# Kernel tuning notes

Hardware: AMD Instinct MI355X
Metric: run time of the kernel (lower is better)

The kernel has to match this reference:

```python
import jax, jax.numpy as jnp
import numpy as np

D_MODEL = 4096
N_HEADS = 32
N_KV_HEADS = 32
D_HEAD = 128
D_LATENT = 512
N_CKV = 4            # n_compressed_kv_heads = d_latent // d_head
T = 2048             # num_tokens (single-sequence prefill)
ROPE_BASE = 10000.0
NEG = -1e30


def _rope(x, positions):
    """Neox-style rotary embedding. x: (T, H, D)."""
    d = x.shape[-1]
    inv_freq = 1.0 / (ROPE_BASE ** (jnp.arange(0, d // 2, dtype=jnp.float32) * (2.0 / d)))
    freqs = positions.astype(jnp.float32)[:, None] * inv_freq[None, :]  # (T, D/2)
    cos = jnp.cos(freqs)[:, None, :]
    sin = jnp.sin(freqs)[:, None, :]
    x1, x2 = jnp.split(x, 2, axis=-1)
    return jnp.concatenate([x1 * cos - x2 * sin, x2 * cos + x1 * sin], axis=-1)


def setup_inputs() -> dict:
    key = jax.random.key(0)
    ks = jax.random.split(key, 6)
    s = jnp.float32(0.02)
    return {
        "positions": jnp.arange(T, dtype=jnp.int32),
        "hidden_states": jax.random.normal(ks[0], (T, D_MODEL), jnp.float32),
        "Wq": jax.random.normal(ks[1], (D_MODEL, N_HEADS * D_HEAD), jnp.float32) * s,
        "Wc": jax.random.normal(ks[2], (D_MODEL, 2 * D_LATENT), jnp.float32) * s,
        "Wuk": jax.random.normal(ks[3], (2 * D_LATENT, N_KV_HEADS * D_HEAD), jnp.float32) * s,
        "Wuv": jax.random.normal(ks[4], (2 * D_LATENT, N_KV_HEADS * D_HEAD), jnp.float32) * s,
        "Wo": jax.random.normal(ks[5], (N_HEADS * D_HEAD, D_MODEL), jnp.float32) * s,
    }


def reference(positions, hidden_states, Wq, Wc, Wuk, Wuv, Wo):
    # Q projection
    q = (hidden_states @ Wq).reshape(T, N_HEADS, D_HEAD)
    # MLA compression: hidden -> c_kv (2*d_latent), split into c_k / c_v
    c_kv = hidden_states @ Wc                                   # (T, 2*D_LATENT)
    c_k = c_kv[:, :D_LATENT].reshape(T, N_CKV, D_HEAD)          # compressed K cache
    c_v = c_kv[:, D_LATENT:].reshape(T, N_CKV, D_HEAD)          # compressed V cache
    # Decompression (computed by the source module; K is RoPE'd then discarded,
    # V is unused -- the v1 attention path runs over the compressed cache).
    K = (c_kv @ Wuk).reshape(T, N_KV_HEADS, D_HEAD)
    V = (c_kv @ Wuv).reshape(T, N_KV_HEADS, D_HEAD)             # noqa: unused, matches source
    # RoPE on q (and K, whose rotated value is dead in the source)
    q = _rope(q, positions)
    K = _rope(K, positions)  # dead, kept for FLOP parity with the source
    # GQA attention: n_heads=32 query heads over n_compressed_kv_heads=4 kv heads
    g = N_HEADS // N_CKV
    qg = q.reshape(T, N_CKV, g, D_HEAD)
    scale = jnp.float32(1.0 / np.sqrt(D_HEAD))
    scores = jnp.einsum('tkgd,skd->kgts', qg, c_k) * scale      # (N_CKV, g, T, T)
    causal = positions[:, None] >= positions[None, :]           # (T, T)
    scores = jnp.where(causal[None, None], scores, NEG)
    probs = jax.nn.softmax(scores, axis=-1)
    ctx = jnp.einsum('kgts,skd->tkgd', probs, c_v).reshape(T, N_HEADS * D_HEAD)
    return ctx @ Wo
```

## Files before the change

### kernel.cpp

```cpp
#include <hip/hip_runtime.h>
#include <hip/hip_bf16.h>
#include <cstdint>
#include <cstddef>


typedef unsigned short u16;
typedef short s16x8 __attribute__((ext_vector_type(8)));
typedef short s16x4 __attribute__((ext_vector_type(4)));
typedef float f32x4 __attribute__((ext_vector_type(4)));

#define MFMA16(a, b, c) __builtin_amdgcn_mfma_f32_16x16x32_bf16((a), (b), (c), 0, 0, 0)

#define QSCALE 0.12751899f
#define LOG2_ROPE_BASE 13.287712379549449f
#define FIXMAX 24.0f

__device__ __forceinline__ u16 f2b(float f) {
  return __builtin_bit_cast(u16, __float2bfloat16(f));
}
__device__ __forceinline__ void async_copy16(u16* lds, const u16* g) {
  __builtin_amdgcn_global_load_lds(
      (const __attribute__((address_space(1))) unsigned int*)g,
      (__attribute__((address_space(3))) unsigned int*)lds, 16, 0, 0);
}

__global__ __launch_bounds__(256)
void prep_kernel(const float* __restrict__ hidden, const float* __restrict__ Wq,
                 const float* __restrict__ Wc, const float* __restrict__ Wo,
                 u16* __restrict__ hb, u16* __restrict__ WqT,
                 u16* __restrict__ WcT, u16* __restrict__ WoT) {
  __shared__ alignas(16) u16 tile[64 * 72];
  const int b = blockIdx.x;
  const int t = threadIdx.x;

  if (b >= 9216) {
    int i = (b - 9216) * 256 + t;
    const float4* p = (const float4*)hidden + (size_t)i * 2;
    float4 a = p[0], c = p[1];
    s16x8 v;
    v[0] = (short)f2b(a.x); v[1] = (short)f2b(a.y);
    v[2] = (short)f2b(a.z); v[3] = (short)f2b(a.w);
    v[4] = (short)f2b(c.x); v[5] = (short)f2b(c.y);
    v[6] = (short)f2b(c.z); v[7] = (short)f2b(c.w);
    *(s16x8*)&hb[(size_t)i * 8] = v;
    return;
  }

  const float* in;
  u16* out;
  int gx, in_ld, out_ld;
  if (b < 4096)      { in = Wq; out = WqT; gx = b;        in_ld = 4096; out_ld = 4096; }
  else if (b < 5120) { in = Wc; out = WcT; gx = b - 4096; in_ld = 1024; out_ld = 4096; }
  else               { in = Wo; out = WoT; gx = b - 5120; in_ld = 4096; out_ld = 4096; }
  const int nbx = in_ld / 64;
  const int c0 = (gx % nbx) * 64, r0 = (gx / nbx) * 64;
  const int rr = t >> 3, cc = (t & 7) * 8;
#pragma unroll
  for (int p = 0; p < 2; p++) {
    int row = p * 32 + rr;
    const float4* src = (const float4*)&in[(size_t)(r0 + row) * in_ld + c0 + cc];
    float4 a = src[0], c = src[1];
    s16x8 v;
    v[0] = (short)f2b(a.x); v[1] = (short)f2b(a.y);
    v[2] = (short)f2b(a.z); v[3] = (short)f2b(a.w);
    v[4] = (short)f2b(c.x); v[5] = (short)f2b(c.y);
    v[6] = (short)f2b(c.z); v[7] = (short)f2b(c.w);
    *(s16x8*)&tile[row * 72 + cc] = v;
  }
  __syncthreads();
#pragma unroll
  for (int p = 0; p < 2; p++) {
    int orow = p * 32 + rr;
    s16x8 v;
#pragma unroll
    for (int j = 0; j < 8; j++) v[j] = (short)tile[(cc + j) * 72 + orow];
    *(s16x8*)&out[(size_t)(c0 + orow) * out_ld + r0 + cc] = v;
  }
}

__global__ __launch_bounds__(256)
void transpose_ckv(const u16* __restrict__ in, u16* __restrict__ out) {
  __shared__ alignas(16) u16 tile[64 * 72];
  const int kh = blockIdx.z;
  const int c0 = blockIdx.x * 64, r0 = blockIdx.y * 64;
  const int in_off = 512 + kh * 128;
  u16* outk = out + (size_t)kh * 128 * 2048;
  const int t = threadIdx.x;
  const int rr = t >> 3, cc = (t & 7) * 8;
#pragma unroll
  for (int p = 0; p < 2; p++) {
    int row = p * 32 + rr;
    s16x8 v = *(const s16x8*)&in[(size_t)(r0 + row) * 1024 + in_off + c0 + cc];
    *(s16x8*)&tile[row * 72 + cc] = v;
  }
  __syncthreads();
#pragma unroll
  for (int p = 0; p < 2; p++) {
    int orow = p * 32 + rr;
    s16x8 v;
#pragma unroll
    for (int j = 0; j < 8; j++) v[j] = (short)tile[(cc + j) * 72 + orow];
    *(s16x8*)&outk[(size_t)(c0 + orow) * 2048 + r0 + cc] = v;
  }
}

template <int EPI>
__global__ __launch_bounds__(256, (EPI == 3) ? 4 : 3)
void gemm_bt(const u16* __restrict__ A, const u16* __restrict__ Bt,
             void* __restrict__ Cv, void* __restrict__ Cv2,
             const int* __restrict__ positions, int kHalf) {
  __shared__ alignas(16) u16 As[128 * 32];
  __shared__ alignas(16) u16 Bs[128 * 32];

  const int tid = threadIdx.x;
  const int w = tid >> 6, l = tid & 63;
  const int wm = w >> 1, wn = w & 1;
  const int lrow = l >> 4, lcol = l & 15;
  const int m0 = blockIdx.y * 128, n0 = blockIdx.x * 128;
  const int k0 = (EPI == 3) ? (int)blockIdx.z * kHalf : 0;
  const int k1 = (EPI == 3) ? k0 + kHalf : 4096;

  f32x4 acc[4][4] = {};

  const int srow = l >> 2;
  const int scol = (l & 3) * 8;
  const u16* Ag = A + (size_t)(m0 + w * 32 + srow) * 4096 + scol;
  const u16* Bg = Bt + (size_t)(n0 + w * 32 + srow) * 4096 + scol;

  for (int kt = k0; kt < k1; kt += 32) {
    __syncthreads();
    async_copy16(&As[(w * 32) * 32], Ag + kt);
    async_copy16(&As[(w * 32 + 16) * 32], Ag + (size_t)16 * 4096 + kt);
    async_copy16(&Bs[(w * 32) * 32], Bg + kt);
    async_copy16(&Bs[(w * 32 + 16) * 32], Bg + (size_t)16 * 4096 + kt);
    __syncthreads();

    s16x8 a[4], b[4];
#pragma unroll
    for (int i = 0; i < 4; i++)
      a[i] = *(const s16x8*)&As[(wm * 64 + i * 16 + lcol) * 32 + lrow * 8];
#pragma unroll
    for (int j = 0; j < 4; j++)
      b[j] = *(const s16x8*)&Bs[(wn * 32 + (j & 1) * 16 + (j >> 1) * 64 + lcol) * 32 +
                                lrow * 8];
#pragma unroll
    for (int i = 0; i < 4; i++)
#pragma unroll
      for (int j = 0; j < 4; j++)
        acc[i][j] = MFMA16(a[i], b[j], acc[i][j]);
  }

  if constexpr (EPI == 3) {
    float* C = (float*)Cv;
#pragma unroll
    for (int i = 0; i < 4; i++) {
      int row = m0 + wm * 64 + i * 16 + lrow * 4;
#pragma unroll
      for (int j = 0; j < 4; j++) {
        int col = n0 + wn * 32 + (j & 1) * 16 + (j >> 1) * 64 + lcol;
#pragma unroll
        for (int r = 0; r < 4; r++)
          atomicAdd(&C[(size_t)(row + r) * 4096 + col], acc[i][j][r]);
      }
    }
  } else {
    if (n0 >= 4096) {
      u16* C = (u16*)Cv2;
      int cb = n0 - 4096;
#pragma unroll
      for (int i = 0; i < 4; i++) {
        int row = m0 + wm * 64 + i * 16 + lrow * 4;
#pragma unroll
        for (int j = 0; j < 4; j++) {
          int col = cb + wn * 32 + (j & 1) * 16 + (j >> 1) * 64 + lcol;
#pragma unroll
          for (int r = 0; r < 4; r++)
            C[(size_t)(row + r) * 1024 + col] = f2b(acc[i][j][r]);
        }
      }
    } else {
      u16* C = (u16*)Cv;
      float inv[2];
#pragma unroll
      for (int j = 0; j < 2; j++) {
        int d = wn * 32 + j * 16 + lcol;
        inv[j] = exp2f((float)d * (-LOG2_ROPE_BASE / 64.f));
      }
#pragma unroll
      for (int i = 0; i < 4; i++) {
        int row = m0 + wm * 64 + i * 16 + lrow * 4;
#pragma unroll
        for (int r = 0; r < 4; r++) {
          float pos = (float)positions[row + r];
#pragma unroll
          for (int j = 0; j < 2; j++) {
            int d = wn * 32 + j * 16 + lcol;
            float ang = pos * inv[j];
            float sv, cv;
            sincosf(ang, &sv, &cv);
            float x1 = acc[i][j][r];
            float x2 = acc[i][j + 2][r];
            C[(size_t)(row + r) * 4096 + n0 + d] = f2b((x1 * cv - x2 * sv) * QSCALE);
            C[(size_t)(row + r) * 4096 + n0 + d + 64] =
                f2b((x2 * cv + x1 * sv) * QSCALE);
          }
        }
      }
    }
  }
}

__global__ __launch_bounds__(256, 3)
void attn_kernel(const u16* __restrict__ Q, const u16* __restrict__ ckv,
                 const u16* __restrict__ vT, u16* __restrict__ ctx) {
  __shared__ alignas(16) u16 S0[16384];
  __shared__ alignas(16) u16 Ps[4][4096];
  __shared__ alignas(16) float red[4][32];

  const int tid = threadIdx.x, w = tid >> 6, l = tid & 63;
  const int lrow = l >> 4, lcol = l & 15;
  const int qt = (int)gridDim.x - 1 - (int)blockIdx.x;
  const int h = blockIdx.y, kh = h >> 3;
  const int q0w = w * 32;

  {
    const u16* qg = Q + (size_t)(qt * 128 + w * 32 + lrow) * 4096 + h * 128 + lcol * 8;
#pragma unroll
    for (int is = 0; is < 8; is++)
      async_copy16(&S0[(w * 32 + is * 4) * 128], qg + (size_t)is * 4 * 4096);
  }
  __syncthreads();
  s16x8 qf[2][4];
#pragma unroll
  for (int nt = 0; nt < 2; nt++)
#pragma unroll
    for (int kc = 0; kc < 4; kc++)
      qf[nt][kc] =
          *(const s16x8*)&S0[(q0w + nt * 16 + lcol) * 128 + kc * 32 + lrow * 8];

  u16* Kt = S0;
  u16* Vt = S0 + 8192;

  f32x4 o[2][8] = {};
  float l_run[2] = {0.f, 0.f};

  const int nkt = 2 * (qt + 1);
  for (int kt = 0; kt < nkt; kt++) {
    __syncthreads();
    {
      const u16* kg =
          ckv + (size_t)(kt * 64 + w * 16 + (l >> 2)) * 1024 + kh * 128 + (l & 3) * 8;
#pragma unroll
      for (int kc = 0; kc < 4; kc++)
        async_copy16(&Kt[kc * 2048 + (w * 16) * 32], kg + kc * 32);
      const u16* vg =
          vT + (size_t)(kh * 128 + w * 32 + (l >> 2)) * 2048 + kt * 64 + (l & 3) * 8;
#pragma unroll
      for (int kc = 0; kc < 2; kc++) {
        async_copy16(&Vt[kc * 4096 + (w * 32) * 32], vg + kc * 32);
        async_copy16(&Vt[kc * 4096 + (w * 32 + 16) * 32],
                     vg + (size_t)16 * 2048 + kc * 32);
      }
    }
    __syncthreads();

    f32x4 s[4][2] = {};
#pragma unroll
    for (int kc = 0; kc < 4; kc++)
#pragma unroll
      for (int mt = 0; mt < 4; mt++) {
        s16x8 ka = *(const s16x8*)&Kt[kc * 2048 + (mt * 16 + lcol) * 32 + lrow * 8];
        s[mt][0] = MFMA16(ka, qf[0][kc], s[mt][0]);
        s[mt][1] = MFMA16(ka, qf[1][kc], s[mt][1]);
      }

    if (kt >= 2 * qt) {
      int koff = (kt & 1) * 64;
#pragma unroll
      for (int mt = 0; mt < 4; mt++)
#pragma unroll
        for (int nt = 0; nt < 2; nt++)
#pragma unroll
          for (int r = 0; r < 4; r++) {
            int key = koff + mt * 16 + lrow * 4 + r;
            int q = q0w + nt * 16 + lcol;
            if (key > q) s[mt][nt][r] = -1e30f;
          }
    }

#pragma unroll
    for (int nt = 0; nt < 2; nt++) {
      float sum = 0.f;
#pragma unroll
      for (int mt = 0; mt < 4; mt++) {
        s16x4 pk;
#pragma unroll
        for (int r = 0; r < 4; r++) {
          float p = exp2f(s[mt][nt][r] - FIXMAX);
          sum += p;
          pk[r] = (short)f2b(p);
        }
        int key = mt * 16 + lrow * 4;
        *(s16x4*)&Ps[w][(key >> 5) * 2048 + (nt * 16 + lcol) * 32 + (key & 31)] = pk;
      }
      sum += __shfl_xor(sum, 16);
      sum += __shfl_xor(sum, 32);
      l_run[nt] += sum;
    }

#pragma unroll
    for (int kc = 0; kc < 2; kc++) {
      s16x8 pa0 = *(const s16x8*)&Ps[w][kc * 2048 + lcol * 32 + lrow * 8];
      s16x8 pa1 = *(const s16x8*)&Ps[w][kc * 2048 + (16 + lcol) * 32 + lrow * 8];
#pragma unroll
      for (int ntO = 0; ntO < 8; ntO++) {
        s16x8 vb = *(const s16x8*)&Vt[kc * 4096 + (ntO * 16 + lcol) * 32 + lrow * 8];
        o[0][ntO] = MFMA16(pa0, vb, o[0][ntO]);
        o[1][ntO] = MFMA16(pa1, vb, o[1][ntO]);
      }
    }
  }

  if (l < 16) {
    red[w][l] = 1.f / l_run[0];
    red[w][16 + l] = 1.f / l_run[1];
  }
  __syncthreads();
  f32x4 lf0 = *(const f32x4*)&red[w][lrow * 4];
  f32x4 lf1 = *(const f32x4*)&red[w][16 + lrow * 4];
#pragma unroll
  for (int mtO = 0; mtO < 2; mtO++)
#pragma unroll
    for (int ntO = 0; ntO < 8; ntO++)
#pragma unroll
      for (int r = 0; r < 4; r++) {
        float lv = mtO ? lf1[r] : lf0[r];
        int q = qt * 128 + q0w + mtO * 16 + lrow * 4 + r;
        int d = h * 128 + ntO * 16 + lcol;
        ctx[(size_t)q * 4096 + d] = f2b(o[mtO][ntO][r] * lv);
      }
}

extern "C" void kernel_launch(void* const* d_in, const int* in_sizes, int n_in,
                              void* d_out, int out_size, void* d_ws, size_t ws_size,
                              hipStream_t stream) {
  const int* positions = (const int*)d_in[0];
  const float* hidden = (const float*)d_in[1];
  const float* Wq = (const float*)d_in[2];
  const float* Wc = (const float*)d_in[3];
  const float* Wo = (const float*)d_in[6];

  char* ws = (char*)d_ws;
  u16* hb  = (u16*)(ws);
  u16* WT  = (u16*)(ws + 16777216);
  u16* qbf = (u16*)(ws + 58720256);
  u16* ckv = (u16*)(ws + 75497472);
  u16* cvT = (u16*)(ws + 79691776);
  u16* WoT = (u16*)(ws + 81788928);
  u16* ctx = hb;

  dim3 blk(256);

  prep_kernel<<<dim3(13312), blk, 0, stream>>>(hidden, Wq, Wc, Wo, hb, WT,
                                               WT + (size_t)4096 * 4096, WoT);

  gemm_bt<1><<<dim3(40, 16), blk, 0, stream>>>(hb, WT, qbf, ckv, positions, 0);

  transpose_ckv<<<dim3(2, 32, 4), blk, 0, stream>>>(ckv, cvT);

  attn_kernel<<<dim3(16, 32), blk, 0, stream>>>(qbf, ckv, cvT, ctx);

  hipMemsetAsync(d_out, 0, (size_t)2048 * 4096 * 4, stream);
  gemm_bt<3><<<dim3(32, 16, 2), blk, 0, stream>>>(ctx, WoT, d_out, nullptr,
                                                  positions, 2048);
}
```

Baseline: 547.7 us.

## Drop split-K in output GEMM and double the K step per sync

The output projection GEMM no longer splits K across two blocks. It stores fp32 results directly, which removes the memset and the atomic adds. Both GEMMs now load two 32-wide K slices per barrier pair, which halves the number of synchronizations and uses twice the LDS per block. The output GEMM runs with half as many blocks, which may lower occupancy and parallelism.

```diff
diff --git a/kernel.cpp b/kernel.cpp
--- a/kernel.cpp
+++ b/kernel.cpp
@@ -105,20 +105,18 @@
 }
 
 template <int EPI>
-__global__ __launch_bounds__(256, (EPI == 3) ? 4 : 3)
+__global__ __launch_bounds__(256, 3)
 void gemm_bt(const u16* __restrict__ A, const u16* __restrict__ Bt,
              void* __restrict__ Cv, void* __restrict__ Cv2,
-             const int* __restrict__ positions, int kHalf) {
-  __shared__ alignas(16) u16 As[128 * 32];
-  __shared__ alignas(16) u16 Bs[128 * 32];
+             const int* __restrict__ positions) {
+  __shared__ alignas(16) u16 As[2][128 * 32];
+  __shared__ alignas(16) u16 Bs[2][128 * 32];
 
   const int tid = threadIdx.x;
   const int w = tid >> 6, l = tid & 63;
   const int wm = w >> 1, wn = w & 1;
   const int lrow = l >> 4, lcol = l & 15;
   const int m0 = blockIdx.y * 128, n0 = blockIdx.x * 128;
-  const int k0 = (EPI == 3) ? (int)blockIdx.z * kHalf : 0;
-  const int k1 = (EPI == 3) ? k0 + kHalf : 4096;
 
   f32x4 acc[4][4] = {};
 
@@ -127,27 +125,35 @@
   const u16* Ag = A + (size_t)(m0 + w * 32 + srow) * 4096 + scol;
   const u16* Bg = Bt + (size_t)(n0 + w * 32 + srow) * 4096 + scol;
 
-  for (int kt = k0; kt < k1; kt += 32) {
+  for (int kt = 0; kt < 4096; kt += 64) {
     __syncthreads();
-    async_copy16(&As[(w * 32) * 32], Ag + kt);
-    async_copy16(&As[(w * 32 + 16) * 32], Ag + (size_t)16 * 4096 + kt);
-    async_copy16(&Bs[(w * 32) * 32], Bg + kt);
-    async_copy16(&Bs[(w * 32 + 16) * 32], Bg + (size_t)16 * 4096 + kt);
+#pragma unroll
+    for (int hf = 0; hf < 2; hf++) {
+      async_copy16(&As[hf][(w * 32) * 32], Ag + kt + hf * 32);
+      async_copy16(&As[hf][(w * 32 + 16) * 32],
+                   Ag + (size_t)16 * 4096 + kt + hf * 32);
+      async_copy16(&Bs[hf][(w * 32) * 32], Bg + kt + hf * 32);
+      async_copy16(&Bs[hf][(w * 32 + 16) * 32],
+                   Bg + (size_t)16 * 4096 + kt + hf * 32);
+    }
     __syncthreads();
 
-    s16x8 a[4], b[4];
-#pragma unroll
-    for (int i = 0; i < 4; i++)
-      a[i] = *(const s16x8*)&As[(wm * 64 + i * 16 + lcol) * 32 + lrow * 8];
-#pragma unroll
-    for (int j = 0; j < 4; j++)
-      b[j] = *(const s16x8*)&Bs[(wn * 32 + (j & 1) * 16 + (j >> 1) * 64 + lcol) * 32 +
-                                lrow * 8];
-#pragma unroll
-    for (int i = 0; i < 4; i++)
+#pragma unroll
+    for (int hf = 0; hf < 2; hf++) {
+      s16x8 a[4], b[4];
+#pragma unroll
+      for (int i = 0; i < 4; i++)
+        a[i] = *(const s16x8*)&As[hf][(wm * 64 + i * 16 + lcol) * 32 + lrow * 8];
 #pragma unroll
       for (int j = 0; j < 4; j++)
-        acc[i][j] = MFMA16(a[i], b[j], acc[i][j]);
+        b[j] = *(const s16x8*)&Bs[hf][(wn * 32 + (j & 1) * 16 + (j >> 1) * 64 +
+                                       lcol) * 32 + lrow * 8];
+#pragma unroll
+      for (int i = 0; i < 4; i++)
+#pragma unroll
+        for (int j = 0; j < 4; j++)
+          acc[i][j] = MFMA16(a[i], b[j], acc[i][j]);
+    }
   }
 
   if constexpr (EPI == 3) {
@@ -160,7 +166,7 @@
         int col = n0 + wn * 32 + (j & 1) * 16 + (j >> 1) * 64 + lcol;
 #pragma unroll
         for (int r = 0; r < 4; r++)
-          atomicAdd(&C[(size_t)(row + r) * 4096 + col], acc[i][j][r]);
+          C[(size_t)(row + r) * 4096 + col] = acc[i][j][r];
       }
     }
   } else {
@@ -364,13 +370,12 @@
   prep_kernel<<<dim3(13312), blk, 0, stream>>>(hidden, Wq, Wc, Wo, hb, WT,
                                                WT + (size_t)4096 * 4096, WoT);
 
-  gemm_bt<1><<<dim3(40, 16), blk, 0, stream>>>(hb, WT, qbf, ckv, positions, 0);
+  gemm_bt<1><<<dim3(40, 16), blk, 0, stream>>>(hb, WT, qbf, ckv, positions);
 
   transpose_ckv<<<dim3(2, 32, 4), blk, 0, stream>>>(ckv, cvT);
 
   attn_kernel<<<dim3(16, 32), blk, 0, stream>>>(qbf, ckv, cvT, ctx);
 
-  hipMemsetAsync(d_out, 0, (size_t)2048 * 4096 * 4, stream);
-  gemm_bt<3><<<dim3(32, 16, 2), blk, 0, stream>>>(ctx, WoT, d_out, nullptr,
-                                                  positions, 2048);
-}
+  gemm_bt<3><<<dim3(32, 16), blk, 0, stream>>>(ctx, WoT, d_out, nullptr,
+                                               positions);
+}
```

After: 507.9 us. 7.3% less time.
